# Kernel optimization log

Measured on AMD Instinct MI355X. Metric: run time of the kernel, lower is better.

## Reference

```python
import jax, jax.numpy as jnp
import numpy as np

_CODESZ = 8
_INT_MAP = (2 ** np.arange(_CODESZ))[::-1].astype(np.int32)  # [128,64,...,1], MSB = dim 0

_NORM12 = np.array([
    [3,1,1,1,3,3,3,3],[1,3,1,1,3,3,3,3],[1,1,3,1,3,3,3,3],[1,1,1,3,3,3,3,3],
    [3,3,3,1,3,3,1,1],[3,3,3,1,3,1,3,1],[3,3,3,1,1,3,3,1],[3,3,3,1,3,1,1,3],
    [3,3,3,1,1,3,1,3],[3,3,3,1,1,1,3,3],[3,3,1,3,3,3,1,1],[3,3,1,3,3,1,3,1],
    [3,3,1,3,1,3,3,1],[3,3,1,3,3,1,1,3],[3,3,1,3,1,3,1,3],[3,3,1,3,1,1,3,3],
    [3,1,3,3,3,3,1,1],[3,1,3,3,3,1,3,1],[3,1,3,3,1,3,3,1],[3,1,3,3,3,1,1,3],
    [3,1,3,3,1,3,1,3],[1,3,3,3,1,1,3,3],[1,3,3,3,3,3,1,1],[1,3,3,3,3,1,3,1],
    [1,3,3,3,1,3,3,1],[1,3,3,3,3,1,1,3],[1,3,3,3,1,3,1,3],[1,3,3,3,1,1,3,3],
    [3,3,1,1,3,3,3,1]], dtype=np.float32) / 2.0


def _build_codebook():
    # abs grid: nonneg half-integer vectors with norm^2 <= 10 == abs of even-sum D8+1/2 shell
    vals = np.array([0.5, 1.5, 2.5], np.float32)  # 3.5^2 > 10, so components <= 2.5
    pts = np.stack(np.meshgrid(*([vals] * _CODESZ), indexing='ij'), -1).reshape(-1, _CODESZ)
    pts = pts[(pts * pts).sum(-1) <= 10.0]                      # 227 rows
    pts = pts[np.lexsort(pts[:, ::-1].T)]                       # torch.unique(dim=0) order
    absg = np.concatenate([pts, _NORM12], 0)                    # [256, 8]

    bits = ((np.arange(256)[:, None] & _INT_MAP[None, :]) > 0).astype(np.int32)  # [256,8]
    pop = bits.sum(-1)
    even_ids = np.where(pop % 2 == 0)[0]                        # 128 even-parity masks
    odd_ids = np.where(pop % 2 == 1)[0]
    signs_even = (1 - 2 * bits[even_ids]).astype(np.float32)    # [128,8]
    signs_odd = (1 - 2 * bits[odd_ids]).astype(np.float32)
    # valid sign parity per abs entry so flipped point has even coordinate sum
    g_even = (absg.sum(-1) % 2.0) == 0.0
    S = np.where(g_even[:, None, None], signs_even[None], signs_odd[None])  # [256,128,8]
    P = (S * absg[:, None, :]).reshape(-1, _CODESZ)             # [32768,8] shell points
    # full grid = [P + 1/4 ; P - 1/4]  (grid[:half] - 1/4 == P, as the module assumes)

    # grid_part: canonical representatives (dims 1: have <=1 negative, min >= -0.5)
    sel = ((P[:, 1:] < 0).sum(-1) <= 1) & (P[:, 1:].min(-1) >= -0.5)
    grid_part = P[sel]                                          # [G,8]
    grid_part_norm = (grid_part * grid_part).sum(-1)            # [G]

    # iterate_mask: even-parity flips x grid_part -> index into grid
    flips = (1 - 2 * bits[even_ids]).astype(np.float32)         # [128,8]
    idx_map = np.zeros(256, np.int32)
    idx_map[even_ids] = np.arange(128, dtype=np.int32)
    gridH = P + 0.25                                            # first half of grid
    gridHn = (gridH * gridH).sum(-1)
    allcombo_idx = np.zeros((128, len(grid_part)), np.int32)
    for i in range(128):  # small fixed loop over sign masks, as in the original
        sc = 2.0 * ((flips[i] * grid_part) @ gridH.T) - gridHn
        allcombo_idx[i] = np.argmax(sc, -1).astype(np.int32)
    # _E8P_GRID_IDX taken as identity permutation -> grid_idx_map = arange - 2^15 (int16)
    grid_idx_map = (np.arange(2 ** 16) - 2 ** 15).astype(np.int16)
    return grid_part, grid_part_norm, allcombo_idx, idx_map, grid_idx_map


def setup_inputs() -> dict:
    key = jax.random.key(0)
    N = 131072
    grid_part, gpn, aci, imap, gim = _build_codebook()
    X = jax.random.normal(key, (N, _CODESZ), dtype=jnp.float32)
    return {
        'X': X,
        'grid_part': jnp.asarray(grid_part),
        'grid_part_norm': jnp.asarray(gpn),
        'allcombo_idx': jnp.asarray(aci),
        'idx_map': jnp.asarray(imap),
        'int_map': jnp.asarray(_INT_MAP),
        'grid_idx_map': jnp.asarray(gim),
    }


def reference(X, grid_part, grid_part_norm, allcombo_idx, idx_map, int_map, grid_idx_map):
    def fast_quantize_part(Y):
        neg = Y < 0                                              # [N,8]
        odd = (neg.sum(-1) % 2) == 1                             # [N] odd # of negatives
        Ya = jnp.abs(Y)
        Ya = Ya.at[:, 0].set(jnp.where(odd, -Ya[:, 0], Ya[:, 0]))
        mask = jnp.where(neg, -1.0, 1.0).astype(Y.dtype)
        mask = mask.at[:, 0].set(jnp.where(odd, -mask[:, 0], mask[:, 0]))
        # nearest codeword: argmax(2 Y.g - |g|^2)  == argmin |Y - g|^2
        q = jnp.argmax(2.0 * (Ya @ grid_part.T) - grid_part_norm, axis=-1)  # [N]
        vals = grid_part[q] * mask
        mint = (((1.0 - mask) * 0.5).astype(jnp.int32) * int_map).sum(-1)   # bit-pack signs
        real_idx = allcombo_idx[idx_map[mint], q]
        err = jnp.sqrt(((Y - vals) ** 2).sum(-1))
        return vals, real_idx, err

    HALF = 2 ** 15
    pv, pi, pe = fast_quantize_part(X + 0.25)
    mv, mi, me = fast_quantize_part(X - 0.25)
    which = pe < me
    final_vals = jnp.where(which[:, None], pv - 0.25, mv + 0.25)
    final_idxs = grid_idx_map[jnp.where(which, pi + HALF, mi)]
    return final_vals, final_idxs
```

## Files before the change

### kernel.cpp

```cpp
#include <hip/hip_runtime.h>
#include <hip/hip_bf16.h>

typedef __attribute__((ext_vector_type(8)))  short bf16x8;
typedef __attribute__((ext_vector_type(16))) float f32x16;

#define TPB 256
#define ERR_MARGIN   1e-4f

static __device__ __forceinline__ unsigned short bf16_rne(float v) {
    union { __hip_bfloat16 h; unsigned short u; } cv;
    cv.h = __float2bfloat16(v);
    return cv.u;
}
static __device__ __forceinline__ float bfhi(unsigned u) { return __uint_as_float(u << 16); }
static __device__ __forceinline__ float bflo(unsigned u) { return __uint_as_float(u & 0xffff0000u); }


__global__ __launch_bounds__(256) void e8p_prep(
    const float* __restrict__ grid_part,
    const float* __restrict__ grid_part_norm,
    unsigned char* __restrict__ ws,
    int G, int T)
{
    __shared__ int cnt[6];
    __shared__ int cur[6];
    const int tid = threadIdx.x;
    const int T32 = T * 32;

    unsigned char* cwB  = ws;
    float*         ngB  = (float*)(ws + (size_t)T32 * 16);
    int*           rmB  = (int*)(ws + (size_t)T32 * 16 + (size_t)T * 32);

    for (int c = tid; c < T32; c += 256) {
        uint4 z; z.x = z.y = z.z = z.w = 0u;
        *(uint4*)(cwB + (size_t)c * 16) = z;
        rmB[c] = -1;
    }
    for (int c = tid; c < T * 8; c += 256) ngB[c] = -30000.0f;
    if (tid < 6) { cnt[tid] = 0; cur[tid] = 0; }
    __syncthreads();

    for (int c = tid; c < G; c += 256) {
        const int k = (__float2int_rn(grid_part_norm[c]) >> 1) - 1;
        atomicAdd(&cnt[k], 1);
    }
    __syncthreads();

    int offs[6];
    {
        int o = 0;
#pragma unroll
        for (int k = 0; k < 6; ++k) { offs[k] = o; o += (cnt[k] + 3) & ~3; }
    }

    for (int c = tid; c < G; c += 256) {
        const int k = (__float2int_rn(grid_part_norm[c]) >> 1) - 1;
        const int pos = offs[k] + atomicAdd(&cur[k], 1);
        const float4 g0 = *(const float4*)(grid_part + (size_t)c * 8);
        const float4 g1 = *(const float4*)(grid_part + (size_t)c * 8 + 4);
        uint4 gv;
        gv.x = (unsigned)bf16_rne(g0.x) | ((unsigned)bf16_rne(g0.y) << 16);
        gv.y = (unsigned)bf16_rne(g0.z) | ((unsigned)bf16_rne(g0.w) << 16);
        gv.z = (unsigned)bf16_rne(g1.x) | ((unsigned)bf16_rne(g1.y) << 16);
        gv.w = (unsigned)bf16_rne(g1.z) | ((unsigned)bf16_rne(g1.w) << 16);
        *(uint4*)(cwB + (size_t)pos * 16) = gv;
        rmB[pos] = c;
    }
    __syncthreads();

    for (int gi = tid; gi < T * 8; gi += 256) {
        const int t = gi >> 3, hh = (gi >> 2) & 1, gg = gi & 3;
        const int p4 = t * 32 + 8 * gg + 4 * hh;
        float v = -30000.0f;
#pragma unroll
        for (int k = 0; k < 6; ++k)
            if (p4 >= offs[k] && p4 < offs[k] + cnt[k]) v = -(float)(k + 1);
        ngB[gi] = v;
    }
}

__global__ __launch_bounds__(TPB, 4) void e8p_fused(
    const float* __restrict__ X,
    const float* __restrict__ grid_part,
    const float* __restrict__ grid_part_norm,
    const int*   __restrict__ allcombo_idx,
    const int*   __restrict__ idx_map,
    const unsigned char* __restrict__ ws,
    float* __restrict__ out,
    int N, int G, int T)
{
    const int T32 = T * 32;
    const int* rmB = (const int*)(ws + (size_t)T32 * 16 + (size_t)T * 32);

    extern __shared__ __align__(16) unsigned char smem[];
    unsigned char* ldsCW = smem;
    float*         ldsNG = (float*)(smem + (size_t)T * 512);

    const int tid = threadIdx.x;
    {
        const uint4* src = (const uint4*)ws;
        uint4* dst = (uint4*)smem;
        const int nchunks = T * 32 + T * 2;
        for (int i = tid; i < nchunks; i += TPB) dst[i] = src[i];
    }
    __syncthreads();

    const int lane = tid & 63;
    const int h    = lane >> 5;
    const int col  = lane & 31;
    const int wave = blockIdx.x * (TPB / 64) + (tid >> 6);

    const int li     = col >> 1;
    const int branch = col & 1;
    const int irow   = wave * 16 + li;
    const int iload  = (irow < N) ? irow : 0;

    float x[8];
    {
        const float4 a = *(const float4*)(X + (size_t)iload * 8);
        const float4 b = *(const float4*)(X + (size_t)iload * 8 + 4);
        x[0]=a.x; x[1]=a.y; x[2]=a.z; x[3]=a.w;
        x[4]=b.x; x[5]=b.y; x[6]=b.z; x[7]=b.w;
    }

    float ya[8]; int neg = 0;
    float sya = 0.0f;
    const float sh = branch ? -0.25f : 0.25f;
#pragma unroll
    for (int j = 0; j < 8; ++j) {
        const float yj = x[j] + sh;
        if (yj < 0.0f) neg |= (1 << (7 - j));
        ya[j] = fabsf(yj);
        sya += fabsf(yj);
    }
    int mint = neg;
    if (__popc(neg) & 1) { ya[0] = -ya[0]; mint ^= 128; }

    const float SM = fmaf(5e-5f, sya, 2e-5f);

    bf16x8 bfrag;
#pragma unroll
    for (int j = 0; j < 8; ++j) {
        const unsigned short hi = bf16_rne(ya[j]);
        const unsigned short lo = bf16_rne(ya[j] - bfhi((unsigned)hi));
        bfrag[j] = (short)(h ? lo : hi);
    }

    float best[4], sec[4]; int qt[4];
#pragma unroll
    for (int g = 0; g < 4; ++g) { best[g] = -1e30f; sec[g] = -1e30f; qt[g] = 0; }

    const unsigned char* aptr = ldsCW + (unsigned)col * 16u;
    const float*         nptr = ldsNG + h * 4;

    const int P = T >> 1;
    bf16x8 a0N = *(const bf16x8*)(aptr);
    bf16x8 a1N = *(const bf16x8*)(aptr + 512);
    float4 n0N = *(const float4*)(nptr);
    float4 n1N = *(const float4*)(nptr + 8);

    const f32x16 czero = {0,0,0,0,0,0,0,0,0,0,0,0,0,0,0,0};
    for (int p = 0; p < P; ++p) {
        const bf16x8 af0 = a0N, af1 = a1N;
        const float4 ng0 = n0N, ng1 = n1N;
        const int pn = (p + 1 < P) ? (p + 1) : p;
        a0N = *(const bf16x8*)(aptr + (size_t)pn * 1024);
        a1N = *(const bf16x8*)(aptr + (size_t)pn * 1024 + 512);
        n0N = *(const float4*)(nptr + (size_t)pn * 16);
        n1N = *(const float4*)(nptr + (size_t)pn * 16 + 8);

        const f32x16 acc0 = __builtin_amdgcn_mfma_f32_32x32x16_bf16(af0, bfrag, czero, 0, 0, 0);
        const f32x16 acc1 = __builtin_amdgcn_mfma_f32_32x32x16_bf16(af1, bfrag, czero, 0, 0, 0);

        const float nga[4] = {ng0.x, ng0.y, ng0.z, ng0.w};
        const float ngb[4] = {ng1.x, ng1.y, ng1.z, ng1.w};
#pragma unroll
        for (int g = 0; g < 4; ++g) {
            const float m = fmaxf(fmaxf(fmaxf(acc0[4*g], acc0[4*g+1]), acc0[4*g+2]),
                                  acc0[4*g+3]);
            const float s = m + nga[g];
            const bool gt = s > best[g];
            sec[g]  = __builtin_amdgcn_fmed3f(s, best[g], sec[g]);
            best[g] = fmaxf(best[g], s);
            qt[g]   = gt ? (2 * p) : qt[g];
        }
#pragma unroll
        for (int g = 0; g < 4; ++g) {
            const float m = fmaxf(fmaxf(fmaxf(acc1[4*g], acc1[4*g+1]), acc1[4*g+2]),
                                  acc1[4*g+3]);
            const float s = m + ngb[g];
            const bool gt = s > best[g];
            sec[g]  = __builtin_amdgcn_fmed3f(s, best[g], sec[g]);
            best[g] = fmaxf(best[g], s);
            qt[g]   = gt ? (2 * p + 1) : qt[g];
        }
    }

    float bb = best[0], ss = sec[0];
    int   ib = (qt[0] << 5) + 4 * h;
#pragma unroll
    for (int g = 1; g < 4; ++g) {
        const int ibg = (qt[g] << 5) + 8 * g + 4 * h;
        const float br = best[g];
        ss = fmaxf(fmaxf(ss, sec[g]), fminf(bb, br));
        const bool take = (br > bb) || ((br == bb) && (ibg < ib));
        bb = fmaxf(bb, br);
        ib = take ? ibg : ib;
    }
    {
        const float ob = __shfl_xor(bb, 32, 64);
        const float os = __shfl_xor(ss, 32, 64);
        const int   oi = __shfl_xor(ib, 32, 64);
        ss = fmaxf(fmaxf(ss, os), fminf(bb, ob));
        const bool take = (ob > bb) || ((ob == bb) && (oi < ib));
        bb = fmaxf(bb, ob);
        ib = take ? oi : ib;
    }

    float hiF[8], loF[8];
#pragma unroll
    for (int j = 0; j < 8; ++j) {
        hiF[j] = bfhi((unsigned)bf16_rne(ya[j]));
        loF[j] = ya[j] - hiF[j];
    }
    const int tW   = ib >> 5;
    const int base = ib & 31;
    const float ngW = ldsNG[tW * 8 + ((base >> 2) & 1) * 4 + (base >> 3)];
    float sm = -1e30f, sec4 = -1e30f; int km = 0;
#pragma unroll
    for (int k = 0; k < 4; ++k) {
        const uint4 gv = *(const uint4*)(ldsCW + ((size_t)tW * 32 + base + k) * 16);
        const float g0 = bfhi(gv.x), g1 = bflo(gv.x), g2 = bfhi(gv.y), g3 = bflo(gv.y);
        const float g4 = bfhi(gv.z), g5 = bflo(gv.z), g6 = bfhi(gv.w), g7 = bflo(gv.w);
        float s = ngW;
        s = fmaf(hiF[0], g0, s); s = fmaf(hiF[1], g1, s);
        s = fmaf(hiF[2], g2, s); s = fmaf(hiF[3], g3, s);
        s = fmaf(hiF[4], g4, s); s = fmaf(hiF[5], g5, s);
        s = fmaf(hiF[6], g6, s); s = fmaf(hiF[7], g7, s);
        s = fmaf(loF[0], g0, s); s = fmaf(loF[1], g1, s);
        s = fmaf(loF[2], g2, s); s = fmaf(loF[3], g3, s);
        s = fmaf(loF[4], g4, s); s = fmaf(loF[5], g5, s);
        s = fmaf(loF[6], g6, s); s = fmaf(loF[7], g7, s);
        const bool gt = s > sm;
        sec4 = __builtin_amdgcn_fmed3f(s, sm, sec4);
        sm   = fmaxf(sm, s);
        km   = gt ? k : km;
    }
    int orig = rmB[tW * 32 + base + km];
    const int closeB = ((sm - sec4) < SM) | ((bb - ss) < SM) | (orig < 0);
    if (orig < 0) orig = 0;

    const int qO     = __shfl_xor(orig, 1, 64);
    const int closeO = __shfl_xor(closeB, 1, 64);
    const int mintO  = __shfl_xor(mint, 1, 64);

    const bool doEpi = (h == 0) && (branch == 0) && (irow < N);
    bool close = false;
    if (doEpi) {
        const int qP = orig, qM = qO;
        const float* gp_ = grid_part + (size_t)qP * 8;
        const float* gm_ = grid_part + (size_t)qM * 8;
        float vp[8], vm[8];
        float ep2 = 0.0f, em2 = 0.0f;
        bool coin = true;
#pragma unroll
        for (int j = 0; j < 8; ++j) {
            const float maskp = ((mint  >> (7 - j)) & 1) ? -1.0f : 1.0f;
            const float maskm = ((mintO >> (7 - j)) & 1) ? -1.0f : 1.0f;
            vp[j] = gp_[j] * maskp;
            vm[j] = gm_[j] * maskm;
            coin = coin && ((vp[j] - 0.25f) == (vm[j] + 0.25f));
            const float dpj = (x[j] + 0.25f) - vp[j];
            const float dmj = (x[j] - 0.25f) - vm[j];
            ep2 = fmaf(dpj, dpj, ep2);
            em2 = fmaf(dmj, dmj, em2);
        }
        close = closeB | closeO | (!coin && (fabsf(ep2 - em2) < ERR_MARGIN));
        if (!close) {
            const bool which = coin ? false : (ep2 < em2);
            const int rowp = idx_map[mint];
            const int rowm = idx_map[mintO];
            const int pi = allcombo_idx[(size_t)rowp * G + qP];
            const int mi = allcombo_idx[(size_t)rowm * G + qM];
            const float idxval = which ? (float)pi : (float)(mi - 32768);
            float* vout = out + (size_t)irow * 8;
#pragma unroll
            for (int j = 0; j < 8; ++j)
                vout[j] = which ? (vp[j] - 0.25f) : (vm[j] + 0.25f);
            out[(size_t)N * 8 + irow] = idxval;
        }
    }

    unsigned long long mb = __ballot(doEpi && close);
    while (mb) {
        const int b = (int)__ffsll(mb) - 1;
        mb &= (mb - 1);
        const int liF = b >> 1;
        const int iF  = wave * 16 + liF;
        float xf[8];
#pragma unroll
        for (int j = 0; j < 8; ++j) xf[j] = __shfl(x[j], b, 64);

        double yapF[8], yamF[8];
        int negp = 0, negm = 0;
#pragma unroll
        for (int j = 0; j < 8; ++j) {
            const double xd = (double)xf[j];
            const double ypd = xd + 0.25;
            const double ymd = xd - 0.25;
            if (ypd < 0.0) negp |= (1 << (7 - j));
            if (ymd < 0.0) negm |= (1 << (7 - j));
            yapF[j] = fabs(ypd);
            yamF[j] = fabs(ymd);
        }
        int mintpF = negp, mintmF = negm;
        if (__popc(negp) & 1) { yapF[0] = -yapF[0]; mintpF ^= 128; }
        if (__popc(negm) & 1) { yamF[0] = -yamF[0]; mintmF ^= 128; }

        double bestpF = -1e300, bestmF = -1e300;
        int qpF = 0x7fffffff, qmF = 0x7fffffff;
        for (int j = lane; j < G; j += 64) {
            const float4 g0 = *(const float4*)(grid_part + (size_t)j * 8);
            const float4 g1 = *(const float4*)(grid_part + (size_t)j * 8 + 4);
            const double n = (double)grid_part_norm[j];
            const double t0 = (double)g0.x, t1 = (double)g0.y,
                         t2 = (double)g0.z, t3 = (double)g0.w,
                         t4 = (double)g1.x, t5 = (double)g1.y,
                         t6 = (double)g1.z, t7 = (double)g1.w;
            double dp, dm;
            dp = yapF[0] * t0;           dm = yamF[0] * t0;
            dp = fma(yapF[1], t1, dp);   dm = fma(yamF[1], t1, dm);
            dp = fma(yapF[2], t2, dp);   dm = fma(yamF[2], t2, dm);
            dp = fma(yapF[3], t3, dp);   dm = fma(yamF[3], t3, dm);
            dp = fma(yapF[4], t4, dp);   dm = fma(yamF[4], t4, dm);
            dp = fma(yapF[5], t5, dp);   dm = fma(yamF[5], t5, dm);
            dp = fma(yapF[6], t6, dp);   dm = fma(yamF[6], t6, dm);
            dp = fma(yapF[7], t7, dp);   dm = fma(yamF[7], t7, dm);
            const double sp = 2.0 * dp - n;
            const double sm2 = 2.0 * dm - n;
            if (sp > bestpF) { bestpF = sp; qpF = j; }
            if (sm2 > bestmF) { bestmF = sm2; qmF = j; }
        }
#pragma unroll
        for (int off = 32; off > 0; off >>= 1) {
            double ob = __shfl_xor(bestpF, off, 64);
            int    oq = __shfl_xor(qpF, off, 64);
            if (ob > bestpF || (ob == bestpF && oq < qpF)) { bestpF = ob; qpF = oq; }
            ob = __shfl_xor(bestmF, off, 64);
            oq = __shfl_xor(qmF, off, 64);
            if (ob > bestmF || (ob == bestmF && oq < qmF)) { bestmF = ob; qmF = oq; }
        }
        if (lane == 0) {
            const float* gp_ = grid_part + (size_t)qpF * 8;
            const float* gm_ = grid_part + (size_t)qmF * 8;
            double vp[8], vm[8];
            double ep2 = 0.0, em2 = 0.0;
#pragma unroll
            for (int j = 0; j < 8; ++j) {
                const double maskp = ((mintpF >> (7 - j)) & 1) ? -1.0 : 1.0;
                const double maskm = ((mintmF >> (7 - j)) & 1) ? -1.0 : 1.0;
                vp[j] = (double)gp_[j] * maskp;
                vm[j] = (double)gm_[j] * maskm;
                const double xd = (double)xf[j];
                const double dpj = (xd + 0.25) - vp[j];
                const double dmj = (xd - 0.25) - vm[j];
                ep2 += dpj * dpj;
                em2 += dmj * dmj;
            }
            const double ep = sqrt(ep2), em = sqrt(em2);
            const bool which = ep < em;
            const int rowp = idx_map[mintpF];
            const int rowm = idx_map[mintmF];
            const int pi = allcombo_idx[(size_t)rowp * G + qpF];
            const int mi = allcombo_idx[(size_t)rowm * G + qmF];
            const float idxval = which ? (float)pi : (float)(mi - 32768);
            float* vout = out + (size_t)iF * 8;
#pragma unroll
            for (int j = 0; j < 8; ++j) {
                const double v = which ? (vp[j] - 0.25) : (vm[j] + 0.25);
                vout[j] = (float)v;
            }
            out[(size_t)N * 8 + iF] = idxval;
        }
    }
}

extern "C" void kernel_launch(void* const* d_in, const int* in_sizes, int n_in,
                              void* d_out, int out_size, void* d_ws, size_t ws_size,
                              hipStream_t stream) {
    const float* X    = (const float*)d_in[0];
    const float* gp   = (const float*)d_in[1];
    const float* gn   = (const float*)d_in[2];
    const int*   aci  = (const int*)d_in[3];
    const int*   imap = (const int*)d_in[4];

    const int N = in_sizes[0] / 8;
    const int G = in_sizes[1] / 8;
    int T = (G + 18 + 31) / 32;
    T += (T & 1);
    const int blocks = (N + 63) / 64;
    const size_t shmem = (size_t)T * 512 + (size_t)T * 32;

    unsigned char* ws = (unsigned char*)d_ws;

    hipLaunchKernelGGL(e8p_prep, dim3(1), dim3(256), 0, stream,
                       gp, gn, ws, G, T);
    hipLaunchKernelGGL(e8p_fused, dim3(blocks), dim3(TPB), shmem, stream,
                       X, gp, gn, aci, imap, ws, (float*)d_out, N, G, T);
}
```

Measured before the change: 123.5 us.

## Fuse codebook prep into main kernel, building sorted LDS codebook per block

Removes the single-block prep kernel and its workspace round trip. Each block now builds the norm-bucketed bf16 codebook, norm table and index map directly in LDS, using ballot/popcount ranking instead of shared atomics so the ordering is deterministic. The row-index lookup moves from global memory to LDS. In exchange every block redoes the codebook construction, reading grid_part from global memory, and uses more LDS, which may reduce occupancy.

```diff
diff --git a/kernel.cpp b/kernel.cpp
--- a/kernel.cpp
+++ b/kernel.cpp
@@ -15,97 +15,99 @@
 static __device__ __forceinline__ float bfhi(unsigned u) { return __uint_as_float(u << 16); }
 static __device__ __forceinline__ float bflo(unsigned u) { return __uint_as_float(u & 0xffff0000u); }
 
-
-__global__ __launch_bounds__(256) void e8p_prep(
-    const float* __restrict__ grid_part,
-    const float* __restrict__ grid_part_norm,
-    unsigned char* __restrict__ ws,
-    int G, int T)
-{
-    __shared__ int cnt[6];
-    __shared__ int cur[6];
-    const int tid = threadIdx.x;
-    const int T32 = T * 32;
-
-    unsigned char* cwB  = ws;
-    float*         ngB  = (float*)(ws + (size_t)T32 * 16);
-    int*           rmB  = (int*)(ws + (size_t)T32 * 16 + (size_t)T * 32);
-
-    for (int c = tid; c < T32; c += 256) {
-        uint4 z; z.x = z.y = z.z = z.w = 0u;
-        *(uint4*)(cwB + (size_t)c * 16) = z;
-        rmB[c] = -1;
-    }
-    for (int c = tid; c < T * 8; c += 256) ngB[c] = -30000.0f;
-    if (tid < 6) { cnt[tid] = 0; cur[tid] = 0; }
-    __syncthreads();
-
-    for (int c = tid; c < G; c += 256) {
-        const int k = (__float2int_rn(grid_part_norm[c]) >> 1) - 1;
-        atomicAdd(&cnt[k], 1);
-    }
-    __syncthreads();
-
-    int offs[6];
-    {
-        int o = 0;
-#pragma unroll
-        for (int k = 0; k < 6; ++k) { offs[k] = o; o += (cnt[k] + 3) & ~3; }
-    }
-
-    for (int c = tid; c < G; c += 256) {
-        const int k = (__float2int_rn(grid_part_norm[c]) >> 1) - 1;
-        const int pos = offs[k] + atomicAdd(&cur[k], 1);
-        const float4 g0 = *(const float4*)(grid_part + (size_t)c * 8);
-        const float4 g1 = *(const float4*)(grid_part + (size_t)c * 8 + 4);
-        uint4 gv;
-        gv.x = (unsigned)bf16_rne(g0.x) | ((unsigned)bf16_rne(g0.y) << 16);
-        gv.y = (unsigned)bf16_rne(g0.z) | ((unsigned)bf16_rne(g0.w) << 16);
-        gv.z = (unsigned)bf16_rne(g1.x) | ((unsigned)bf16_rne(g1.y) << 16);
-        gv.w = (unsigned)bf16_rne(g1.z) | ((unsigned)bf16_rne(g1.w) << 16);
-        *(uint4*)(cwB + (size_t)pos * 16) = gv;
-        rmB[pos] = c;
-    }
-    __syncthreads();
-
-    for (int gi = tid; gi < T * 8; gi += 256) {
-        const int t = gi >> 3, hh = (gi >> 2) & 1, gg = gi & 3;
-        const int p4 = t * 32 + 8 * gg + 4 * hh;
-        float v = -30000.0f;
-#pragma unroll
-        for (int k = 0; k < 6; ++k)
-            if (p4 >= offs[k] && p4 < offs[k] + cnt[k]) v = -(float)(k + 1);
-        ngB[gi] = v;
-    }
-}
-
 __global__ __launch_bounds__(TPB, 4) void e8p_fused(
     const float* __restrict__ X,
     const float* __restrict__ grid_part,
     const float* __restrict__ grid_part_norm,
     const int*   __restrict__ allcombo_idx,
     const int*   __restrict__ idx_map,
-    const unsigned char* __restrict__ ws,
     float* __restrict__ out,
     int N, int G, int T)
 {
     const int T32 = T * 32;
-    const int* rmB = (const int*)(ws + (size_t)T32 * 16 + (size_t)T * 32);
-
     extern __shared__ __align__(16) unsigned char smem[];
     unsigned char* ldsCW = smem;
     float*         ldsNG = (float*)(smem + (size_t)T * 512);
-
-    const int tid = threadIdx.x;
+    int*           ldsI  = (int*)(smem + (size_t)T * 512 + (size_t)T * 32);
+
+    __shared__ int cntS[12][4][6];
+    __shared__ int totS[6];
+
+    const int tid    = threadIdx.x;
+    const int lane   = tid & 63;
+    const int waveid = tid >> 6;
+    const int nch    = (G + TPB - 1) / TPB;
+
+    for (int c = tid; c < T32; c += TPB) {
+        uint4 z; z.x = z.y = z.z = z.w = 0u;
+        *(uint4*)(ldsCW + (size_t)c * 16) = z;
+        ldsI[c] = -1;
+    }
+    for (int m = 0; m < nch; ++m) {
+        const int c = m * TPB + tid;
+        int k = 6;
+        if (c < G) k = (__float2int_rn(grid_part_norm[c]) >> 1) - 1;
+#pragma unroll
+        for (int kk = 0; kk < 6; ++kk) {
+            const unsigned long long mask = __ballot(k == kk);
+            if (lane == 0) cntS[m][waveid][kk] = (int)__popcll(mask);
+        }
+    }
+    __syncthreads();
+    if (tid < 6) {
+        const int kk = tid;
+        int run = 0;
+        for (int m = 0; m < nch; ++m)
+            for (int w = 0; w < 4; ++w) {
+                const int v = cntS[m][w][kk];
+                cntS[m][w][kk] = run;
+                run += v;
+            }
+        totS[kk] = run;
+    }
+    __syncthreads();
+    int offs[6];
     {
-        const uint4* src = (const uint4*)ws;
-        uint4* dst = (uint4*)smem;
-        const int nchunks = T * 32 + T * 2;
-        for (int i = tid; i < nchunks; i += TPB) dst[i] = src[i];
+        int o = 0;
+#pragma unroll
+        for (int kk = 0; kk < 6; ++kk) { offs[kk] = o; o += (totS[kk] + 3) & ~3; }
+    }
+    for (int m = 0; m < nch; ++m) {
+        const int c = m * TPB + tid;
+        int k = 6;
+        if (c < G) k = (__float2int_rn(grid_part_norm[c]) >> 1) - 1;
+        unsigned long long mymask = 0;
+#pragma unroll
+        for (int kk = 0; kk < 6; ++kk) {
+            const unsigned long long mask = __ballot(k == kk);
+            if (kk == k) mymask = mask;
+        }
+        if (c < G) {
+            const int rank = cntS[m][waveid][k] +
+                             (int)__popcll(mymask & ((1ull << lane) - 1ull));
+            const int pos = offs[k] + rank;
+            const float4 g0 = *(const float4*)(grid_part + (size_t)c * 8);
+            const float4 g1 = *(const float4*)(grid_part + (size_t)c * 8 + 4);
+            uint4 gv;
+            gv.x = (unsigned)bf16_rne(g0.x) | ((unsigned)bf16_rne(g0.y) << 16);
+            gv.y = (unsigned)bf16_rne(g0.z) | ((unsigned)bf16_rne(g0.w) << 16);
+            gv.z = (unsigned)bf16_rne(g1.x) | ((unsigned)bf16_rne(g1.y) << 16);
+            gv.w = (unsigned)bf16_rne(g1.z) | ((unsigned)bf16_rne(g1.w) << 16);
+            *(uint4*)(ldsCW + (size_t)pos * 16) = gv;
+            ldsI[pos] = c;
+        }
+    }
+    for (int gi = tid; gi < T * 8; gi += TPB) {
+        const int t = gi >> 3, hh = (gi >> 2) & 1, gg = gi & 3;
+        const int p4 = t * 32 + 8 * gg + 4 * hh;
+        float v = -30000.0f;
+#pragma unroll
+        for (int kk = 0; kk < 6; ++kk)
+            if (p4 >= offs[kk] && p4 < offs[kk] + totS[kk]) v = -(float)(kk + 1);
+        ldsNG[gi] = v;
     }
     __syncthreads();
 
-    const int lane = tid & 63;
     const int h    = lane >> 5;
     const int col  = lane & 31;
     const int wave = blockIdx.x * (TPB / 64) + (tid >> 6);
@@ -246,7 +248,7 @@
         sm   = fmaxf(sm, s);
         km   = gt ? k : km;
     }
-    int orig = rmB[tW * 32 + base + km];
+    int orig = ldsI[tW * 32 + base + km];
     const int closeB = ((sm - sec4) < SM) | ((bb - ss) < SM) | (orig < 0);
     if (orig < 0) orig = 0;
 
@@ -399,12 +401,8 @@
     int T = (G + 18 + 31) / 32;
     T += (T & 1);
     const int blocks = (N + 63) / 64;
-    const size_t shmem = (size_t)T * 512 + (size_t)T * 32;
-
-    unsigned char* ws = (unsigned char*)d_ws;
-
-    hipLaunchKernelGGL(e8p_prep, dim3(1), dim3(256), 0, stream,
-                       gp, gn, ws, G, T);
+    const size_t shmem = (size_t)T * 512 + (size_t)T * 32 + (size_t)T * 128;
+
     hipLaunchKernelGGL(e8p_fused, dim3(blocks), dim3(TPB), shmem, stream,
-                       X, gp, gn, aci, imap, ws, (float*)d_out, N, G, T);
+                       X, gp, gn, aci, imap, (float*)d_out, N, G, T);
 }
```

Measured after the change: 128.6 us. +4.1%, slower.
